# Performance work log

Measured on AMD Instinct MI355X. Metric: run time of the kernel, lower is better.

The kernel has to match this reference:

```python
import jax, jax.numpy as jnp
import numpy as np

N_NODES = 50000
N_EDGES = 500000
IN_FEATS = 96
OUT_FEATS = 128
N_ETYPES = 4
N_STEPS = 3  # feat is never updated (no GRU), so each step is identical


def setup_inputs() -> dict:
    key = jax.random.key(0)
    k1, k2, k3, k4, k5 = jax.random.split(key, 5)
    feat = jax.random.normal(k1, (N_NODES, IN_FEATS), dtype=jnp.float32)
    etypes = jax.random.randint(k2, (N_EDGES,), 0, N_ETYPES, dtype=jnp.int64)
    src = jax.random.randint(k3, (N_EDGES,), 0, N_NODES, dtype=jnp.int64)
    dst = jax.random.randint(k4, (N_EDGES,), 0, N_NODES, dtype=jnp.int64)
    # per-etype Linear(out_feats, out_feats): W[i] is [out, out], xavier-normal-ish
    gain = float(np.sqrt(2.0))  # calculate_gain('relu')
    std = gain * np.sqrt(2.0 / (OUT_FEATS + OUT_FEATS))
    W = jax.random.normal(k5, (N_ETYPES, OUT_FEATS, OUT_FEATS), dtype=jnp.float32) * std
    b = jnp.zeros((N_ETYPES, OUT_FEATS), dtype=jnp.float32)
    return {"feat": feat, "etypes": etypes, "src": src, "dst": dst, "W": W, "b": b}


def reference(feat, etypes, src, dst, W, b):
    n_nodes = feat.shape[0]
    # h_i^0 = [x_i || 0]  -> pad to out_feats
    h = jnp.pad(feat, ((0, 0), (0, OUT_FEATS - feat.shape[1])))  # [N, out]
    # Since there is no GRU, h never changes across n_steps; each step's 'a'
    # is identical, so one aggregation suffices (faithful to returned value).
    h_src = h[src]  # [E, out] gather
    msgs = jnp.zeros((h_src.shape[0], OUT_FEATS), dtype=h.dtype)
    for i in range(N_ETYPES):
        # Linear: x @ W_i^T + b_i, applied only to edges of type i
        m_i = h_src @ W[i].T + b[i]  # [E, out]
        msgs = jnp.where((etypes == i)[:, None], m_i, msgs)
    # scatter-sum messages to destination nodes
    a = jax.ops.segment_sum(msgs, dst, num_segments=n_nodes)  # [N, out]
    return a
```

## Files before the change

kernel.cpp:

```cpp
#include <hip/hip_runtime.h>
#include <hip/hip_bf16.h>

#define N_NODES 50000
#define N_EDGES 500000
#define IN_FEATS 96
#define OUT_FEATS 128
#define N_ETYPES 4
#define KCAT (N_ETYPES * IN_FEATS)

typedef __attribute__((ext_vector_type(8))) short short8;
typedef __attribute__((ext_vector_type(4))) short short4v;
typedef __attribute__((ext_vector_type(4))) float f32x4;

static __device__ inline short f2bf_bits(float f) {
    __hip_bfloat16 h = __float2bfloat16(f);
    return *reinterpret_cast<short*>(&h);
}
static __device__ inline unsigned pack2bf(float lo, float hi) {
    unsigned l = (unsigned short)f2bf_bits(lo);
    unsigned h = (unsigned short)f2bf_bits(hi);
    return l | (h << 16);
}

__global__ __launch_bounds__(256) void k_hist(const int* __restrict__ dst, int* __restrict__ deg) {
    int e = blockIdx.x * 256 + threadIdx.x;
    if (e < N_EDGES) atomicAdd(&deg[dst[e]], 1);
}

__global__ __launch_bounds__(256) void k_scan1(const int* __restrict__ in, int n,
                                               int* __restrict__ out, int* __restrict__ bsum) {
    int g = blockIdx.x * 256 + threadIdx.x;
    int lane = threadIdx.x & 63, wave = threadIdx.x >> 6;
    int v = (g < n) ? in[g] : 0;
    int orig = v;
    for (int off = 1; off < 64; off <<= 1) {
        int u = __shfl_up(v, off);
        if (lane >= off) v += u;
    }
    __shared__ int wsum[4];
    if (lane == 63) wsum[wave] = v;
    __syncthreads();
    if (threadIdx.x == 0) {
        int s = 0;
        for (int w = 0; w < 4; ++w) { int t = wsum[w]; wsum[w] = s; s += t; }
        bsum[blockIdx.x] = s;
    }
    __syncthreads();
    int excl = v - orig + wsum[wave];
    if (g < n) out[g] = excl;
}

__global__ __launch_bounds__(256) void k_scan3(int* __restrict__ pos, const int* __restrict__ bscan,
                                               int* __restrict__ cursor, int n) {
    int g = blockIdx.x * 256 + threadIdx.x;
    if (g < n) {
        int p = pos[g] + bscan[blockIdx.x];
        pos[g] = p;
        cursor[g] = p;
    }
}

__global__ __launch_bounds__(256) void k_bin(const int* __restrict__ dst, const int* __restrict__ src,
                                             const int* __restrict__ etypes,
                                             int* __restrict__ cursor, int* __restrict__ packed) {
    int e = blockIdx.x * 256 + threadIdx.x;
    if (e < N_EDGES) {
        int slot = atomicAdd(&cursor[dst[e]], 1);
        packed[slot] = src[e] | (etypes[e] << 16);
    }
}

__global__ __launch_bounds__(64) void k_agg(const float2* __restrict__ feat2,
                                            const int* __restrict__ pos, const int* __restrict__ deg,
                                            const int* __restrict__ packed,
                                            unsigned* __restrict__ Scat_u32,
                                            float* __restrict__ counts) {
    const int d = blockIdx.x;
    const int lane = threadIdx.x;
    const bool act = lane < 48;
    const int start = pos[d], cnt = deg[d];

    float2 a0 = {0.f, 0.f}, a1 = {0.f, 0.f}, a2 = {0.f, 0.f}, a3 = {0.f, 0.f};
    int c0 = 0, c1 = 0, c2 = 0, c3 = 0;
    const float2 zero = {0.f, 0.f};

    int i = 0;
    for (; i + 4 <= cnt; i += 4) {
        int p0 = packed[start + i + 0];
        int p1 = packed[start + i + 1];
        int p2 = packed[start + i + 2];
        int p3 = packed[start + i + 3];
        float2 v0 = act ? feat2[(size_t)(p0 & 0xFFFF) * 48 + lane] : zero;
        float2 v1 = act ? feat2[(size_t)(p1 & 0xFFFF) * 48 + lane] : zero;
        float2 v2 = act ? feat2[(size_t)(p2 & 0xFFFF) * 48 + lane] : zero;
        float2 v3 = act ? feat2[(size_t)(p3 & 0xFFFF) * 48 + lane] : zero;
        int e0 = p0 >> 16, e1 = p1 >> 16, e2 = p2 >> 16, e3 = p3 >> 16;
        if (e0 == 0) { a0.x += v0.x; a0.y += v0.y; ++c0; }
        else if (e0 == 1) { a1.x += v0.x; a1.y += v0.y; ++c1; }
        else if (e0 == 2) { a2.x += v0.x; a2.y += v0.y; ++c2; }
        else              { a3.x += v0.x; a3.y += v0.y; ++c3; }
        if (e1 == 0) { a0.x += v1.x; a0.y += v1.y; ++c0; }
        else if (e1 == 1) { a1.x += v1.x; a1.y += v1.y; ++c1; }
        else if (e1 == 2) { a2.x += v1.x; a2.y += v1.y; ++c2; }
        else              { a3.x += v1.x; a3.y += v1.y; ++c3; }
        if (e2 == 0) { a0.x += v2.x; a0.y += v2.y; ++c0; }
        else if (e2 == 1) { a1.x += v2.x; a1.y += v2.y; ++c1; }
        else if (e2 == 2) { a2.x += v2.x; a2.y += v2.y; ++c2; }
        else              { a3.x += v2.x; a3.y += v2.y; ++c3; }
        if (e3 == 0) { a0.x += v3.x; a0.y += v3.y; ++c0; }
        else if (e3 == 1) { a1.x += v3.x; a1.y += v3.y; ++c1; }
        else if (e3 == 2) { a2.x += v3.x; a2.y += v3.y; ++c2; }
        else              { a3.x += v3.x; a3.y += v3.y; ++c3; }
    }
    for (; i < cnt; ++i) {
        int p = packed[start + i];
        float2 v = act ? feat2[(size_t)(p & 0xFFFF) * 48 + lane] : zero;
        int e = p >> 16;
        if (e == 0) { a0.x += v.x; a0.y += v.y; ++c0; }
        else if (e == 1) { a1.x += v.x; a1.y += v.y; ++c1; }
        else if (e == 2) { a2.x += v.x; a2.y += v.y; ++c2; }
        else              { a3.x += v.x; a3.y += v.y; ++c3; }
    }

    if (act) {
        size_t base = (size_t)d * (KCAT / 2) + lane;
        Scat_u32[base]           = pack2bf(a0.x, a0.y);
        Scat_u32[base + 48]      = pack2bf(a1.x, a1.y);
        Scat_u32[base + 96]      = pack2bf(a2.x, a2.y);
        Scat_u32[base + 144]     = pack2bf(a3.x, a3.y);
    }
    if (lane < 4) counts[d * 4 + lane] = (float)(lane == 0 ? c0 : lane == 1 ? c1 : lane == 2 ? c2 : c3);
}

#define LDT 104

__global__ __launch_bounds__(256) void k_gemm(const __hip_bfloat16* __restrict__ Scat,
                                              const float* __restrict__ W,
                                              const float* __restrict__ b,
                                              const float* __restrict__ counts,
                                              float* __restrict__ out) {
    __shared__ __align__(16) __hip_bfloat16 As[128][LDT];
    __shared__ __align__(16) __hip_bfloat16 Bs[128][LDT];
    const int m0 = blockIdx.x * 128;
    const int tid = threadIdx.x, lane = tid & 63, wave = tid >> 6;
    const int wm = wave >> 1, wn = wave & 1;

    f32x4 acc[4][4];
#pragma unroll
    for (int i = 0; i < 4; ++i)
#pragma unroll
        for (int jj = 0; jj < 4; ++jj) acc[i][jj] = (f32x4){0.f, 0.f, 0.f, 0.f};

    for (int ks = 0; ks < 4; ++ks) {
#pragma unroll
        for (int it = 0; it < 6; ++it) {
            int idx = tid + it * 256;
            int row = idx / 12, c8 = idx % 12;
            int gm = m0 + row;
            if (gm > N_NODES - 1) gm = N_NODES - 1;
            short8 v = *reinterpret_cast<const short8*>(&Scat[(size_t)gm * KCAT + ks * IN_FEATS + c8 * 8]);
            *reinterpret_cast<short8*>(&As[row][c8 * 8]) = v;
        }
#pragma unroll
        for (int it = 0; it < 12; ++it) {
            int idx = tid + it * 256;
            int row = idx / 24, c4 = idx % 24;
            float4 v = *reinterpret_cast<const float4*>(&W[(size_t)(ks * OUT_FEATS + row) * OUT_FEATS + c4 * 4]);
            short4v sv;
            sv[0] = f2bf_bits(v.x); sv[1] = f2bf_bits(v.y);
            sv[2] = f2bf_bits(v.z); sv[3] = f2bf_bits(v.w);
            *reinterpret_cast<short4v*>(&Bs[row][c4 * 4]) = sv;
        }
        __syncthreads();
#pragma unroll
        for (int kk = 0; kk < 3; ++kk) {
            short8 af[4], bf[4];
#pragma unroll
            for (int mi = 0; mi < 4; ++mi)
                af[mi] = *reinterpret_cast<const short8*>(&As[wm * 64 + mi * 16 + (lane & 15)][kk * 32 + (lane >> 4) * 8]);
#pragma unroll
            for (int ni = 0; ni < 4; ++ni)
                bf[ni] = *reinterpret_cast<const short8*>(&Bs[wn * 64 + ni * 16 + (lane & 15)][kk * 32 + (lane >> 4) * 8]);
#pragma unroll
            for (int mi = 0; mi < 4; ++mi)
#pragma unroll
                for (int ni = 0; ni < 4; ++ni)
                    acc[mi][ni] = __builtin_amdgcn_mfma_f32_16x16x32_bf16(af[mi], bf[ni], acc[mi][ni], 0, 0, 0);
        }
        __syncthreads();
    }

#pragma unroll
    for (int mi = 0; mi < 4; ++mi) {
#pragma unroll
        for (int r = 0; r < 4; ++r) {
            int m = m0 + wm * 64 + mi * 16 + (lane >> 4) * 4 + r;
            if (m < N_NODES) {
                float4 c4 = *reinterpret_cast<const float4*>(&counts[m * 4]);
#pragma unroll
                for (int ni = 0; ni < 4; ++ni) {
                    int n = wn * 64 + ni * 16 + (lane & 15);
                    float bias = c4.x * b[n] + c4.y * b[OUT_FEATS + n] +
                                 c4.z * b[2 * OUT_FEATS + n] + c4.w * b[3 * OUT_FEATS + n];
                    out[(size_t)m * OUT_FEATS + n] = acc[mi][ni][r] + bias;
                }
            }
        }
    }
}

__global__ __launch_bounds__(256) void edge_direct(const float* __restrict__ feat,
                                                   const int* __restrict__ etypes,
                                                   const int* __restrict__ src,
                                                   const int* __restrict__ dst,
                                                   const float* __restrict__ W,
                                                   const float* __restrict__ b,
                                                   float* __restrict__ out) {
    int gid = blockIdx.x * 256 + threadIdx.x;
    int e = gid >> 7;
    int j = gid & 127;
    if (e >= N_EDGES) return;
    int et = etypes[e];
    int s = src[e];
    int d = dst[e];
    const float* f = feat + (size_t)s * IN_FEATS;
    const float* w = W + ((size_t)et * OUT_FEATS + j) * OUT_FEATS;
    float acc = b[et * OUT_FEATS + j];
    for (int k = 0; k < IN_FEATS; ++k) acc += f[k] * w[k];
    atomicAdd(&out[(size_t)d * OUT_FEATS + j], acc);
}

extern "C" void kernel_launch(void* const* d_in, const int* in_sizes, int n_in,
                              void* d_out, int out_size, void* d_ws, size_t ws_size,
                              hipStream_t stream) {
    const float* feat  = (const float*)d_in[0];
    const int*   etyps = (const int*)d_in[1];
    const int*   src   = (const int*)d_in[2];
    const int*   dst   = (const int*)d_in[3];
    const float* W     = (const float*)d_in[4];
    const float* b     = (const float*)d_in[5];
    float* out = (float*)d_out;

    const size_t off_scat   = 0;
    const size_t off_counts = off_scat + (size_t)N_NODES * KCAT * 2;
    const size_t off_deg    = off_counts + (size_t)N_NODES * 4 * 4;
    const size_t off_pos    = off_deg + (size_t)N_NODES * 4;
    const size_t off_cursor = off_pos + (size_t)N_NODES * 4;
    const size_t off_packed = off_cursor + (size_t)N_NODES * 4;
    const size_t off_bsum   = off_packed + (size_t)N_EDGES * 4;
    const size_t off_bscan  = off_bsum + 1024;
    const size_t off_scrap  = off_bscan + 1024;
    const size_t need = off_scrap + 1024;

    if (ws_size >= need) {
        char* ws = (char*)d_ws;
        __hip_bfloat16* Scat = (__hip_bfloat16*)(ws + off_scat);
        unsigned* Scat_u32 = (unsigned*)(ws + off_scat);
        float* counts = (float*)(ws + off_counts);
        int* deg    = (int*)(ws + off_deg);
        int* pos    = (int*)(ws + off_pos);
        int* cursor = (int*)(ws + off_cursor);
        int* packed = (int*)(ws + off_packed);
        int* bsum   = (int*)(ws + off_bsum);
        int* bscan  = (int*)(ws + off_bscan);
        int* scrap  = (int*)(ws + off_scrap);

        const int nScanBlocks = (N_NODES + 255) / 256;

        hipMemsetAsync(deg, 0, (size_t)N_NODES * 4, stream);
        k_hist<<<(N_EDGES + 255) / 256, 256, 0, stream>>>(dst, deg);
        k_scan1<<<nScanBlocks, 256, 0, stream>>>(deg, N_NODES, pos, bsum);
        k_scan1<<<1, 256, 0, stream>>>(bsum, nScanBlocks, bscan, scrap);
        k_scan3<<<nScanBlocks, 256, 0, stream>>>(pos, bscan, cursor, N_NODES);
        k_bin<<<(N_EDGES + 255) / 256, 256, 0, stream>>>(dst, src, etyps, cursor, packed);
        k_agg<<<N_NODES, 64, 0, stream>>>((const float2*)feat, pos, deg, packed, Scat_u32, counts);
        k_gemm<<<(N_NODES + 127) / 128, 256, 0, stream>>>(Scat, W, b, counts, out);
    } else {
        hipMemsetAsync(d_out, 0, (size_t)out_size * sizeof(float), stream);
        int nthreads = N_EDGES * OUT_FEATS;
        edge_direct<<<nthreads / 256, 256, 0, stream>>>(feat, etyps, src, dst, W, b, out);
    }
}
```

Measured before the change: 119.9 us.

## Precompute bf16 weights once and record atomic ranks to drop binning atomics

```diff
diff --git a/kernel.cpp b/kernel.cpp
--- a/kernel.cpp
+++ b/kernel.cpp
@@ -9,7 +9,6 @@
 #define KCAT (N_ETYPES * IN_FEATS)
 
 typedef __attribute__((ext_vector_type(8))) short short8;
-typedef __attribute__((ext_vector_type(4))) short short4v;
 typedef __attribute__((ext_vector_type(4))) float f32x4;
 
 static __device__ inline short f2bf_bits(float f) {
@@ -22,9 +21,24 @@
     return l | (h << 16);
 }
 
-__global__ __launch_bounds__(256) void k_hist(const int* __restrict__ dst, int* __restrict__ deg) {
+__global__ __launch_bounds__(256) void k_init(int* __restrict__ deg,
+                                              const float* __restrict__ W,
+                                              unsigned* __restrict__ Wb_u32) {
+    int g = blockIdx.x * 256 + threadIdx.x;
+    if (g < N_NODES) deg[g] = 0;
+    if (g < 512 * 48) {
+        int row = g / 48, pair = g % 48;
+        float lo = W[(size_t)row * OUT_FEATS + pair * 2];
+        float hi = W[(size_t)row * OUT_FEATS + pair * 2 + 1];
+        Wb_u32[g] = pack2bf(lo, hi);
+    }
+}
+
+__global__ __launch_bounds__(256) void k_hist(const int* __restrict__ dst,
+                                              int* __restrict__ deg,
+                                              int* __restrict__ rank) {
     int e = blockIdx.x * 256 + threadIdx.x;
-    if (e < N_EDGES) atomicAdd(&deg[dst[e]], 1);
+    if (e < N_EDGES) rank[e] = atomicAdd(&deg[dst[e]], 1);
 }
 
 __global__ __launch_bounds__(256) void k_scan1(const int* __restrict__ in, int n,
@@ -50,22 +64,18 @@
     if (g < n) out[g] = excl;
 }
 
-__global__ __launch_bounds__(256) void k_scan3(int* __restrict__ pos, const int* __restrict__ bscan,
-                                               int* __restrict__ cursor, int n) {
+__global__ __launch_bounds__(256) void k_scan3(int* __restrict__ pos, const int* __restrict__ bscan, int n) {
     int g = blockIdx.x * 256 + threadIdx.x;
-    if (g < n) {
-        int p = pos[g] + bscan[blockIdx.x];
-        pos[g] = p;
-        cursor[g] = p;
-    }
+    if (g < n) pos[g] += bscan[blockIdx.x];
 }
 
 __global__ __launch_bounds__(256) void k_bin(const int* __restrict__ dst, const int* __restrict__ src,
                                              const int* __restrict__ etypes,
-                                             int* __restrict__ cursor, int* __restrict__ packed) {
+                                             const int* __restrict__ pos, const int* __restrict__ rank,
+                                             int* __restrict__ packed) {
     int e = blockIdx.x * 256 + threadIdx.x;
     if (e < N_EDGES) {
-        int slot = atomicAdd(&cursor[dst[e]], 1);
+        int slot = pos[dst[e]] + rank[e];
         packed[slot] = src[e] | (etypes[e] << 16);
     }
 }
@@ -124,10 +134,10 @@
 
     if (act) {
         size_t base = (size_t)d * (KCAT / 2) + lane;
-        Scat_u32[base]           = pack2bf(a0.x, a0.y);
-        Scat_u32[base + 48]      = pack2bf(a1.x, a1.y);
-        Scat_u32[base + 96]      = pack2bf(a2.x, a2.y);
-        Scat_u32[base + 144]     = pack2bf(a3.x, a3.y);
+        Scat_u32[base]       = pack2bf(a0.x, a0.y);
+        Scat_u32[base + 48]  = pack2bf(a1.x, a1.y);
+        Scat_u32[base + 96]  = pack2bf(a2.x, a2.y);
+        Scat_u32[base + 144] = pack2bf(a3.x, a3.y);
     }
     if (lane < 4) counts[d * 4 + lane] = (float)(lane == 0 ? c0 : lane == 1 ? c1 : lane == 2 ? c2 : c3);
 }
@@ -135,7 +145,7 @@
 #define LDT 104
 
 __global__ __launch_bounds__(256) void k_gemm(const __hip_bfloat16* __restrict__ Scat,
-                                              const float* __restrict__ W,
+                                              const short* __restrict__ Wb,
                                               const float* __restrict__ b,
                                               const float* __restrict__ counts,
                                               float* __restrict__ out) {
@@ -162,14 +172,11 @@
             *reinterpret_cast<short8*>(&As[row][c8 * 8]) = v;
         }
 #pragma unroll
-        for (int it = 0; it < 12; ++it) {
+        for (int it = 0; it < 6; ++it) {
             int idx = tid + it * 256;
-            int row = idx / 24, c4 = idx % 24;
-            float4 v = *reinterpret_cast<const float4*>(&W[(size_t)(ks * OUT_FEATS + row) * OUT_FEATS + c4 * 4]);
-            short4v sv;
-            sv[0] = f2bf_bits(v.x); sv[1] = f2bf_bits(v.y);
-            sv[2] = f2bf_bits(v.z); sv[3] = f2bf_bits(v.w);
-            *reinterpret_cast<short4v*>(&Bs[row][c4 * 4]) = sv;
+            int row = idx / 12, c8 = idx % 12;
+            short8 v = *reinterpret_cast<const short8*>(&Wb[((size_t)ks * OUT_FEATS + row) * IN_FEATS + c8 * 8]);
+            *reinterpret_cast<short8*>(&Bs[row][c8 * 8]) = v;
         }
         __syncthreads();
 #pragma unroll
@@ -245,12 +252,13 @@
     const size_t off_counts = off_scat + (size_t)N_NODES * KCAT * 2;
     const size_t off_deg    = off_counts + (size_t)N_NODES * 4 * 4;
     const size_t off_pos    = off_deg + (size_t)N_NODES * 4;
-    const size_t off_cursor = off_pos + (size_t)N_NODES * 4;
-    const size_t off_packed = off_cursor + (size_t)N_NODES * 4;
+    const size_t off_rank   = off_pos + (size_t)N_NODES * 4;
+    const size_t off_packed = off_rank + (size_t)N_EDGES * 4;
     const size_t off_bsum   = off_packed + (size_t)N_EDGES * 4;
     const size_t off_bscan  = off_bsum + 1024;
     const size_t off_scrap  = off_bscan + 1024;
-    const size_t need = off_scrap + 1024;
+    const size_t off_wb     = off_scrap + 1024;
+    const size_t need = off_wb + (size_t)512 * IN_FEATS * 2;
 
     if (ws_size >= need) {
         char* ws = (char*)d_ws;
@@ -259,22 +267,25 @@
         float* counts = (float*)(ws + off_counts);
         int* deg    = (int*)(ws + off_deg);
         int* pos    = (int*)(ws + off_pos);
-        int* cursor = (int*)(ws + off_cursor);
+        int* rank   = (int*)(ws + off_rank);
         int* packed = (int*)(ws + off_packed);
         int* bsum   = (int*)(ws + off_bsum);
         int* bscan  = (int*)(ws + off_bscan);
         int* scrap  = (int*)(ws + off_scrap);
+        unsigned* Wb_u32 = (unsigned*)(ws + off_wb);
+        short* Wb = (short*)(ws + off_wb);
 
         const int nScanBlocks = (N_NODES + 255) / 256;
-
-        hipMemsetAsync(deg, 0, (size_t)N_NODES * 4, stream);
-        k_hist<<<(N_EDGES + 255) / 256, 256, 0, stream>>>(dst, deg);
+        const int nEdgeBlocks = (N_EDGES + 255) / 256;
+
+        k_init<<<nScanBlocks, 256, 0, stream>>>(deg, W, Wb_u32);
+        k_hist<<<nEdgeBlocks, 256, 0, stream>>>(dst, deg, rank);
         k_scan1<<<nScanBlocks, 256, 0, stream>>>(deg, N_NODES, pos, bsum);
         k_scan1<<<1, 256, 0, stream>>>(bsum, nScanBlocks, bscan, scrap);
-        k_scan3<<<nScanBlocks, 256, 0, stream>>>(pos, bscan, cursor, N_NODES);
-        k_bin<<<(N_EDGES + 255) / 256, 256, 0, stream>>>(dst, src, etyps, cursor, packed);
+        k_scan3<<<nScanBlocks, 256, 0, stream>>>(pos, bscan, N_NODES);
+        k_bin<<<nEdgeBlocks, 256, 0, stream>>>(dst, src, etyps, pos, rank, packed);
         k_agg<<<N_NODES, 64, 0, stream>>>((const float2*)feat, pos, deg, packed, Scat_u32, counts);
-        k_gemm<<<(N_NODES + 127) / 128, 256, 0, stream>>>(Scat, W, b, counts, out);
+        k_gemm<<<(N_NODES + 127) / 128, 256, 0, stream>>>(Scat, Wb, b, counts, out);
     } else {
         hipMemsetAsync(d_out, 0, (size_t)out_size * sizeof(float), stream);
         int nthreads = N_EDGES * OUT_FEATS;
```

Result: faster. 100.2 us (-16.4%).
